# Performance work log

Hardware: AMD Instinct MI355X
Metric: run time of the kernel (lower is better)

The kernel has to match this reference:

```python
import jax, jax.numpy as jnp
import numpy as np


def setup_inputs() -> dict:
    key = jax.random.key(0)
    ks = jax.random.split(key, 6)
    B, C, H, W, K = 4, 64, 352, 1216, 3
    OC = K * K - 1  # 8 guide channels from convbn
    return {
        "feature": jax.random.normal(ks[0], (B, C, H, W), jnp.float32),
        "conv_w": jax.random.normal(ks[1], (OC, C, 3, 3), jnp.float32) * 0.05,
        "gamma": jax.random.uniform(ks[2], (OC,), jnp.float32, 0.5, 1.5),
        "beta": jax.random.normal(ks[3], (OC,), jnp.float32) * 0.1,
        "mean": jax.random.normal(ks[4], (OC,), jnp.float32) * 0.1,
        "var": jax.random.uniform(ks[5], (OC,), jnp.float32, 0.5, 1.5),
        "kernel_size": K,
    }


def reference(feature, conv_w, gamma, beta, mean, var, kernel_size):
    k = kernel_size
    eps = 1e-5
    # conv 3x3, stride 1, pad 1, no bias  -> [B, k*k-1, H, W]
    x = jax.lax.conv_general_dilated(
        feature, conv_w, window_strides=(1, 1), padding=((1, 1), (1, 1)),
        dimension_numbers=("NCHW", "OIHW", "NCHW"))
    c = lambda v: v[None, :, None, None]
    # BatchNorm2d in eval mode (running stats + affine)
    guide = (x - c(mean)) * (c(gamma) * jax.lax.rsqrt(c(var) + eps)) + c(beta)
    # L1-normalize across channels, middle weight = 1 - sum of the others
    gsum = jnp.sum(jnp.abs(guide), axis=1, keepdims=True)
    guide = guide / gsum
    guide_mid = 1.0 - jnp.sum(guide, axis=1, keepdims=True)
    mid = (k * k - 1) // 2
    # per-offset zero-pad each single channel into [H+k-1, W+k-1] canvas
    pads = []
    for t in range(k * k):  # fixed small loop over kernel offsets (k*k = 9)
        i, j = t // k, t % k  # top=i, bottom=k-1-i, left=j, right=k-1-j
        if t < mid:
            ch = guide[:, t:t + 1]
        elif t > mid:
            ch = guide[:, t - 1:t]
        else:
            ch = guide_mid
        pads.append(jnp.pad(ch, ((0, 0), (0, 0), (i, k - 1 - i), (j, k - 1 - j))))
    return jnp.concatenate(pads, axis=1)  # [B, k*k, H+k-1, W+k-1]
```

## Files before the change

### kernel.cpp

```cpp
#include <hip/hip_runtime.h>
#include <hip/hip_bf16.h>

#define BATCH 4
#define CIN 64
#define HH 352
#define WW 1216
#define OCH 8
#define OHH 354
#define OWW 1218
#define HW (HH * WW)

#define BH 16
#define BW 32
#define FR 18
#define FC 34
#define NPOS (FR * FC)
#define NTHR 256
#define NIT 10
#define GX 38
#define GY 22
#define NWG (GX * GY * BATCH)
#define CPX (NWG / 8)

typedef short bf16x8 __attribute__((ext_vector_type(8)));
typedef float f32x4  __attribute__((ext_vector_type(4)));

static __device__ __forceinline__ unsigned f2bf(float x) {
    unsigned u = __float_as_uint(x);
    return (u + 0x7FFFu + ((u >> 16) & 1u)) >> 16;
}

__global__ void repack_kernel(const float* __restrict__ conv_w,
                              const float* __restrict__ gamma,
                              const float* __restrict__ beta,
                              const float* __restrict__ mean,
                              const float* __restrict__ var,
                              unsigned short* __restrict__ wB,
                              float* __restrict__ bias)
{
    int tid = blockIdx.x * 256 + threadIdx.x;
    if (tid < 18 * 64) {
        int tc = tid >> 6;
        int lane = tid & 63;
        int tap = tc >> 1, cc = tc & 1;
        int oc = lane & 15, hi = lane >> 4;
        unsigned v[8];
#pragma unroll
        for (int j = 0; j < 8; ++j) {
            float w = 0.f;
            if (oc < 8) {
                int c = cc * 32 + hi * 8 + j;
                float scl = gamma[oc] * rsqrtf(var[oc] + 1e-5f);
                w = conv_w[((size_t)oc * CIN + c) * 9 + tap] * scl;
            }
            v[j] = f2bf(w);
        }
        uint4 pk;
        pk.x = v[0] | (v[1] << 16);
        pk.y = v[2] | (v[3] << 16);
        pk.z = v[4] | (v[5] << 16);
        pk.w = v[6] | (v[7] << 16);
        ((uint4*)wB)[tid] = pk;
    }
    if (tid < OCH) {
        float scl = gamma[tid] * rsqrtf(var[tid] + 1e-5f);
        bias[tid] = beta[tid] - mean[tid] * scl;
    }
}

__global__ void border_kernel(float* __restrict__ out)
{
    const int bt = blockIdx.x;
    const int t = bt % 9;
    const int i = t / 3, j = t % 3;
    float* pl = out + (size_t)bt * OHH * OWW;
    const int r0 = (i == 0) ? HH : 0;
    const int r1 = (i == 2) ? 1 : (OHH - 1);
    const int c0 = (j == 0) ? WW : 0;
    const int c1 = (j == 2) ? 1 : (OWW - 1);
    const int nrow = 2 * OWW;
    for (int idx = threadIdx.x; idx < 2 * OWW + 2 * OHH; idx += blockDim.x) {
        if (idx < nrow) {
            int r = (idx < OWW) ? r0 : r1;
            int c = (idx < OWW) ? idx : idx - OWW;
            pl[(size_t)r * OWW + c] = 0.f;
        } else {
            int k = idx - nrow;
            int c = (k < OHH) ? c0 : c1;
            int r = (k < OHH) ? k : k - OHH;
            pl[(size_t)r * OWW + c] = 0.f;
        }
    }
}

__global__ __launch_bounds__(NTHR, 2)
void conv_mfma(const float* __restrict__ feature,
               const unsigned short* __restrict__ wB,
               const float* __restrict__ bias,
               float* __restrict__ out)
{
    __shared__ uint4 sF[NPOS * 4];

    const int lin = blockIdx.x;
    const int wg  = (lin & 7) * CPX + (lin >> 3);
    const int bx  = wg % GX;
    const int byz = wg / GX;
    const int by  = byz % GY;
    const int b   = byz / GY;

    const int tid  = threadIdx.x;
    const int wave = tid >> 6;
    const int lane = tid & 63;
    const int oc   = lane & 15;
    const int hi   = lane >> 4;
    const int h0 = by * BH;
    const int w0 = bx * BW;

    const float* fb = feature + (size_t)b * CIN * HW;
    const int soct = tid & 3;
    const int p0   = tid >> 2;

    f32x4 acc[4][2];
#pragma unroll
    for (int rr = 0; rr < 4; ++rr)
#pragma unroll
        for (int cg = 0; cg < 2; ++cg) acc[rr][cg] = (f32x4)0.f;

#pragma unroll 1
    for (int cc = 0; cc < 2; ++cc) {
        if (cc) __syncthreads();
        const float* chbase = fb + (size_t)(cc * 32 + soct * 8) * HW;
        float v[NIT][8];
        float msk[NIT];
        int   cps[NIT];
#pragma unroll
        for (int it = 0; it < NIT; ++it) {
            int pos = p0 + it * 64;
            int cp = (pos < NPOS) ? pos : (NPOS - 1);
            int fr = cp / FC;
            int fc = cp - fr * FC;
            int gh = h0 - 1 + fr, gw = w0 - 1 + fc;
            bool ok = ((unsigned)gh < (unsigned)HH) && ((unsigned)gw < (unsigned)WW);
            int sgh = min(max(gh, 0), HH - 1);
            int sgw = min(max(gw, 0), WW - 1);
            const float* sp = chbase + sgh * WW + sgw;
#pragma unroll
            for (int j = 0; j < 8; ++j) v[it][j] = sp[(size_t)j * HW];
            msk[it] = ok ? 1.f : 0.f;
            cps[it] = cp;
        }
        bf16x8 bwl[9];
#pragma unroll
        for (int t = 0; t < 9; ++t)
            bwl[t] = ((const bf16x8*)wB)[(t * 2 + cc) * 64 + lane];
#pragma unroll
        for (int it = 0; it < NIT; ++it) {
            float mk = msk[it];
            uint4 pk;
            pk.x = f2bf(v[it][0] * mk) | (f2bf(v[it][1] * mk) << 16);
            pk.y = f2bf(v[it][2] * mk) | (f2bf(v[it][3] * mk) << 16);
            pk.z = f2bf(v[it][4] * mk) | (f2bf(v[it][5] * mk) << 16);
            pk.w = f2bf(v[it][6] * mk) | (f2bf(v[it][7] * mk) << 16);
            int cp = cps[it];
            sF[cp * 4 + (soct ^ ((cp >> 1) & 3))] = pk;
        }
        __syncthreads();
#pragma unroll
        for (int t = 0; t < 9; ++t) {
            const int dh = t / 3, dw = t % 3;
#pragma unroll
            for (int rr = 0; rr < 4; ++rr) {
                const int fr = wave * 4 + rr + dh;
#pragma unroll
                for (int cg = 0; cg < 2; ++cg) {
                    const int fc = cg * 16 + oc + dw;
                    const int pp = fr * FC + fc;
                    bf16x8 av = *reinterpret_cast<const bf16x8*>(&sF[pp * 4 + (hi ^ ((pp >> 1) & 3))]);
                    acc[rr][cg] = __builtin_amdgcn_mfma_f32_16x16x32_bf16(av, bwl[t], acc[rr][cg], 0, 0, 0);
                }
            }
        }
    }

    const float myb = (oc < 8) ? bias[oc] : 0.f;
    const int t = (oc < 8) ? ((oc < 4) ? oc : oc + 1) : 4;
    const bool dow = (oc <= 8);
    const int ii = t / 3, jj = t % 3;
    float* pl = out + ((size_t)(b * 9 + t) * OHH + ii) * OWW + jj;

#pragma unroll
    for (int rr = 0; rr < 4; ++rr) {
        const int h = h0 + wave * 4 + rr;
#pragma unroll
        for (int cg = 0; cg < 2; ++cg) {
#pragma unroll
            for (int reg = 0; reg < 4; ++reg) {
                float vv = acc[rr][cg][reg] + myb;
                float av = fabsf(vv);
                float sv = vv;
                av += __shfl_xor(av, 1);  sv += __shfl_xor(sv, 1);
                av += __shfl_xor(av, 2);  sv += __shfl_xor(sv, 2);
                av += __shfl_xor(av, 4);  sv += __shfl_xor(sv, 4);
                av += __shfl_xor(av, 8);  sv += __shfl_xor(sv, 8);
                float inv = 1.0f / av;
                float val = (oc == 8) ? (1.0f - sv * inv) : (vv * inv);
                if (dow) {
                    int w = w0 + cg * 16 + hi * 4 + reg;
                    pl[(size_t)h * OWW + w] = val;
                }
            }
        }
    }
}

extern "C" void kernel_launch(void* const* d_in, const int* in_sizes, int n_in,
                              void* d_out, int out_size, void* d_ws, size_t ws_size,
                              hipStream_t stream) {
    const float* feature = (const float*)d_in[0];
    const float* conv_w  = (const float*)d_in[1];
    const float* gamma   = (const float*)d_in[2];
    const float* beta    = (const float*)d_in[3];
    const float* mean    = (const float*)d_in[4];
    const float* var     = (const float*)d_in[5];
    float* out = (float*)d_out;

    unsigned short* wB = (unsigned short*)d_ws;
    float* bias = (float*)((char*)d_ws + 18432);

    border_kernel<<<BATCH * 9, 256, 0, stream>>>(out);
    repack_kernel<<<5, 256, 0, stream>>>(conv_w, gamma, beta, mean, var, wB, bias);
    conv_mfma<<<NWG, NTHR, 0, stream>>>(feature, wB, bias, out);
}
```

Measured before the change: 219.9 us.

## Give each wave a private LDS halo tile and drop block barriers

Each wave now stages its own 6-row halo window (its 4 output rows plus 2 halo rows) into a private LDS slot, so the two __syncthreads per channel chunk are removed. Loads are split into three smaller passes to cap register use. The cost is redundant global reads and bf16 conversion of overlapping halo rows (6 rows per 4 instead of 18 per 16), plus more LDS per block, which may reduce occupancy.

```diff
diff --git a/kernel.cpp b/kernel.cpp
--- a/kernel.cpp
+++ b/kernel.cpp
@@ -12,11 +12,11 @@
 
 #define BH 16
 #define BW 32
-#define FR 18
 #define FC 34
-#define NPOS (FR * FC)
+#define WROWS 6
+#define WPOS (WROWS * FC)
+#define WSLOT (WPOS * 4)
 #define NTHR 256
-#define NIT 10
 #define GX 38
 #define GY 22
 #define NWG (GX * GY * BATCH)
@@ -93,13 +93,37 @@
     }
 }
 
+#define STAGE_PASS(Q0, NP) { \
+    float v[NP][8]; float mk[NP]; int sl[NP]; \
+    _Pragma("unroll") for (int k = 0; k < NP; ++k) { \
+        int pos = p0 + (Q0 + k) * 16; \
+        pos = (pos < WPOS) ? pos : (WPOS - 1);           \
+        int lr = pos / FC; int fc = pos - lr * FC; \
+        int gh = h0w - 1 + lr, gw = w0 - 1 + fc; \
+        bool ok = ((unsigned)gh < (unsigned)HH) && ((unsigned)gw < (unsigned)WW); \
+        int sgh = min(max(gh, 0), HH - 1); \
+        int sgw = min(max(gw, 0), WW - 1); \
+        const float* sp = chbase + sgh * WW + sgw; \
+        _Pragma("unroll") for (int j = 0; j < 8; ++j) v[k][j] = sp[(size_t)j * HW]; \
+        mk[k] = ok ? 1.f : 0.f; \
+        sl[k] = wslot0 + pos * 4 + (soct ^ ((pos >> 1) & 3)); \
+    } \
+    _Pragma("unroll") for (int k = 0; k < NP; ++k) { \
+        float m_ = mk[k]; uint4 pk; \
+        pk.x = f2bf(v[k][0] * m_) | (f2bf(v[k][1] * m_) << 16); \
+        pk.y = f2bf(v[k][2] * m_) | (f2bf(v[k][3] * m_) << 16); \
+        pk.z = f2bf(v[k][4] * m_) | (f2bf(v[k][5] * m_) << 16); \
+        pk.w = f2bf(v[k][6] * m_) | (f2bf(v[k][7] * m_) << 16); \
+        sF[sl[k]] = pk; \
+    } }
+
 __global__ __launch_bounds__(NTHR, 2)
 void conv_mfma(const float* __restrict__ feature,
                const unsigned short* __restrict__ wB,
                const float* __restrict__ bias,
                float* __restrict__ out)
 {
-    __shared__ uint4 sF[NPOS * 4];
+    __shared__ uint4 sF[4 * WSLOT];
 
     const int lin = blockIdx.x;
     const int wg  = (lin & 7) * CPX + (lin >> 3);
@@ -115,10 +139,12 @@
     const int hi   = lane >> 4;
     const int h0 = by * BH;
     const int w0 = bx * BW;
+    const int h0w = h0 + wave * 4;
+    const int wslot0 = wave * WSLOT;
 
     const float* fb = feature + (size_t)b * CIN * HW;
-    const int soct = tid & 3;
-    const int p0   = tid >> 2;
+    const int soct = lane & 3;
+    const int p0   = lane >> 2;
 
     f32x4 acc[4][2];
 #pragma unroll
@@ -128,54 +154,29 @@
 
 #pragma unroll 1
     for (int cc = 0; cc < 2; ++cc) {
-        if (cc) __syncthreads();
         const float* chbase = fb + (size_t)(cc * 32 + soct * 8) * HW;
-        float v[NIT][8];
-        float msk[NIT];
-        int   cps[NIT];
-#pragma unroll
-        for (int it = 0; it < NIT; ++it) {
-            int pos = p0 + it * 64;
-            int cp = (pos < NPOS) ? pos : (NPOS - 1);
-            int fr = cp / FC;
-            int fc = cp - fr * FC;
-            int gh = h0 - 1 + fr, gw = w0 - 1 + fc;
-            bool ok = ((unsigned)gh < (unsigned)HH) && ((unsigned)gw < (unsigned)WW);
-            int sgh = min(max(gh, 0), HH - 1);
-            int sgw = min(max(gw, 0), WW - 1);
-            const float* sp = chbase + sgh * WW + sgw;
-#pragma unroll
-            for (int j = 0; j < 8; ++j) v[it][j] = sp[(size_t)j * HW];
-            msk[it] = ok ? 1.f : 0.f;
-            cps[it] = cp;
-        }
+
+        STAGE_PASS(0, 5)
+        STAGE_PASS(5, 4)
+        STAGE_PASS(9, 4)
+
         bf16x8 bwl[9];
 #pragma unroll
         for (int t = 0; t < 9; ++t)
             bwl[t] = ((const bf16x8*)wB)[(t * 2 + cc) * 64 + lane];
-#pragma unroll
-        for (int it = 0; it < NIT; ++it) {
-            float mk = msk[it];
-            uint4 pk;
-            pk.x = f2bf(v[it][0] * mk) | (f2bf(v[it][1] * mk) << 16);
-            pk.y = f2bf(v[it][2] * mk) | (f2bf(v[it][3] * mk) << 16);
-            pk.z = f2bf(v[it][4] * mk) | (f2bf(v[it][5] * mk) << 16);
-            pk.w = f2bf(v[it][6] * mk) | (f2bf(v[it][7] * mk) << 16);
-            int cp = cps[it];
-            sF[cp * 4 + (soct ^ ((cp >> 1) & 3))] = pk;
-        }
-        __syncthreads();
+
 #pragma unroll
         for (int t = 0; t < 9; ++t) {
             const int dh = t / 3, dw = t % 3;
 #pragma unroll
             for (int rr = 0; rr < 4; ++rr) {
-                const int fr = wave * 4 + rr + dh;
+                const int lr = rr + dh;
 #pragma unroll
                 for (int cg = 0; cg < 2; ++cg) {
                     const int fc = cg * 16 + oc + dw;
-                    const int pp = fr * FC + fc;
-                    bf16x8 av = *reinterpret_cast<const bf16x8*>(&sF[pp * 4 + (hi ^ ((pp >> 1) & 3))]);
+                    const int pp = lr * FC + fc;
+                    bf16x8 av = *reinterpret_cast<const bf16x8*>(
+                        &sF[wslot0 + pp * 4 + (hi ^ ((pp >> 1) & 3))]);
                     acc[rr][cg] = __builtin_amdgcn_mfma_f32_16x16x32_bf16(av, bwl[t], acc[rr][cg], 0, 0, 0);
                 }
             }
@@ -190,7 +191,7 @@
 
 #pragma unroll
     for (int rr = 0; rr < 4; ++rr) {
-        const int h = h0 + wave * 4 + rr;
+        const int h = h0w + rr;
 #pragma unroll
         for (int cg = 0; cg < 2; ++cg) {
 #pragma unroll
```

Result: slower. 263.7 us (+19.9%).

## Double-buffer LDS and prefetch second channel chunk during first MFMA pass

Applied to the files above, without the earlier changes.

The conv kernel now keeps two LDS buffers, one per 32-channel chunk. The first chunk is loaded in two halves and staged, then the global loads for the second chunk are issued into registers before the first chunk's MFMAs run, so memory latency overlaps with compute. The second chunk is packed into the other buffer afterwards, which removes one barrier. In exchange the kernel holds 80 floats of prefetch in registers during the MFMA loop and doubles LDS use, which may cause spills or lower occupancy under launch_bounds(256,2).

```diff
diff --git a/kernel.cpp b/kernel.cpp
--- a/kernel.cpp
+++ b/kernel.cpp
@@ -93,13 +93,34 @@
     }
 }
 
+#define PACK1(VV, MK, SL, BUF) { \
+    uint4 pk_; \
+    pk_.x = f2bf(VV[0] * MK) | (f2bf(VV[1] * MK) << 16); \
+    pk_.y = f2bf(VV[2] * MK) | (f2bf(VV[3] * MK) << 16); \
+    pk_.z = f2bf(VV[4] * MK) | (f2bf(VV[5] * MK) << 16); \
+    pk_.w = f2bf(VV[6] * MK) | (f2bf(VV[7] * MK) << 16); \
+    (BUF)[SL] = pk_; }
+
+#define MFMA_CHUNK(BUF) \
+    _Pragma("unroll") for (int t = 0; t < 9; ++t) { \
+        const int dh = t / 3, dw = t % 3; \
+        _Pragma("unroll") for (int rr = 0; rr < 4; ++rr) { \
+            const int fr = wv4 + rr + dh; \
+            _Pragma("unroll") for (int cg = 0; cg < 2; ++cg) { \
+                const int fc = cg * 16 + oc + dw; \
+                const int pp = fr * FC + fc; \
+                bf16x8 av = *reinterpret_cast<const bf16x8*>(&(BUF)[pp * 4 + (hi ^ ((pp >> 1) & 3))]); \
+                acc[rr][cg] = __builtin_amdgcn_mfma_f32_16x16x32_bf16(av, bwl[t], acc[rr][cg], 0, 0, 0); \
+            } } }
+
 __global__ __launch_bounds__(NTHR, 2)
 void conv_mfma(const float* __restrict__ feature,
                const unsigned short* __restrict__ wB,
                const float* __restrict__ bias,
                float* __restrict__ out)
 {
-    __shared__ uint4 sF[NPOS * 4];
+    __shared__ uint4 sA[NPOS * 4];
+    __shared__ uint4 sB[NPOS * 4];
 
     const int lin = blockIdx.x;
     const int wg  = (lin & 7) * CPX + (lin >> 3);
@@ -113,6 +134,7 @@
     const int lane = tid & 63;
     const int oc   = lane & 15;
     const int hi   = lane >> 4;
+    const int wv4  = wave * 4;
     const int h0 = by * BH;
     const int w0 = bx * BW;
 
@@ -126,60 +148,64 @@
 #pragma unroll
         for (int cg = 0; cg < 2; ++cg) acc[rr][cg] = (f32x4)0.f;
 
+    {
+        const float* chbase = fb + (size_t)(soct * 8) * HW;
 #pragma unroll 1
-    for (int cc = 0; cc < 2; ++cc) {
-        if (cc) __syncthreads();
-        const float* chbase = fb + (size_t)(cc * 32 + soct * 8) * HW;
-        float v[NIT][8];
-        float msk[NIT];
-        int   cps[NIT];
+        for (int hf = 0; hf < 2; ++hf) {
+            float v[5][8]; float mk5[5]; int sl5[5];
+#pragma unroll
+            for (int k = 0; k < 5; ++k) {
+                int it = hf * 5 + k;
+                int pos2 = p0 + it * 64; pos2 = (pos2 < NPOS) ? pos2 : (NPOS - 1);
+                int fr2 = pos2 / FC; int fc2 = pos2 - fr2 * FC;
+                int gh2 = h0 - 1 + fr2, gw2 = w0 - 1 + fc2;
+                mk5[k] = (((unsigned)gh2 < (unsigned)HH) && ((unsigned)gw2 < (unsigned)WW)) ? 1.f : 0.f;
+                sl5[k] = pos2 * 4 + (soct ^ ((pos2 >> 1) & 3));
+                const float* sp2 = chbase + (min(max(gh2, 0), HH - 1) * WW + min(max(gw2, 0), WW - 1));
+#pragma unroll
+                for (int j = 0; j < 8; ++j) v[k][j] = sp2[(size_t)j * HW];
+            }
+#pragma unroll
+            for (int k = 0; k < 5; ++k) PACK1(v[k], mk5[k], sl5[k], sA)
+        }
+    }
+    __syncthreads();
+
+    float v1[NIT][8]; float mk1[NIT]; int sl1[NIT];
+    {
+        const float* chbase = fb + (size_t)(32 + soct * 8) * HW;
 #pragma unroll
         for (int it = 0; it < NIT; ++it) {
-            int pos = p0 + it * 64;
-            int cp = (pos < NPOS) ? pos : (NPOS - 1);
-            int fr = cp / FC;
-            int fc = cp - fr * FC;
-            int gh = h0 - 1 + fr, gw = w0 - 1 + fc;
-            bool ok = ((unsigned)gh < (unsigned)HH) && ((unsigned)gw < (unsigned)WW);
-            int sgh = min(max(gh, 0), HH - 1);
-            int sgw = min(max(gw, 0), WW - 1);
-            const float* sp = chbase + sgh * WW + sgw;
-#pragma unroll
-            for (int j = 0; j < 8; ++j) v[it][j] = sp[(size_t)j * HW];
-            msk[it] = ok ? 1.f : 0.f;
-            cps[it] = cp;
-        }
+            int pos2 = p0 + it * 64; pos2 = (pos2 < NPOS) ? pos2 : (NPOS - 1);
+            int fr2 = pos2 / FC; int fc2 = pos2 - fr2 * FC;
+            int gh2 = h0 - 1 + fr2, gw2 = w0 - 1 + fc2;
+            mk1[it] = (((unsigned)gh2 < (unsigned)HH) && ((unsigned)gw2 < (unsigned)WW)) ? 1.f : 0.f;
+            sl1[it] = pos2 * 4 + (soct ^ ((pos2 >> 1) & 3));
+            const float* sp2 = chbase + (min(max(gh2, 0), HH - 1) * WW + min(max(gw2, 0), WW - 1));
+#pragma unroll
+            for (int j = 0; j < 8; ++j) v1[it][j] = sp2[(size_t)j * HW];
+        }
+    }
+    __builtin_amdgcn_sched_barrier(0);
+
+    {
         bf16x8 bwl[9];
 #pragma unroll
         for (int t = 0; t < 9; ++t)
-            bwl[t] = ((const bf16x8*)wB)[(t * 2 + cc) * 64 + lane];
-#pragma unroll
-        for (int it = 0; it < NIT; ++it) {
-            float mk = msk[it];
-            uint4 pk;
-            pk.x = f2bf(v[it][0] * mk) | (f2bf(v[it][1] * mk) << 16);
-            pk.y = f2bf(v[it][2] * mk) | (f2bf(v[it][3] * mk) << 16);
-            pk.z = f2bf(v[it][4] * mk) | (f2bf(v[it][5] * mk) << 16);
-            pk.w = f2bf(v[it][6] * mk) | (f2bf(v[it][7] * mk) << 16);
-            int cp = cps[it];
-            sF[cp * 4 + (soct ^ ((cp >> 1) & 3))] = pk;
-        }
-        __syncthreads();
-#pragma unroll
-        for (int t = 0; t < 9; ++t) {
-            const int dh = t / 3, dw = t % 3;
-#pragma unroll
-            for (int rr = 0; rr < 4; ++rr) {
-                const int fr = wave * 4 + rr + dh;
-#pragma unroll
-                for (int cg = 0; cg < 2; ++cg) {
-                    const int fc = cg * 16 + oc + dw;
-                    const int pp = fr * FC + fc;
-                    bf16x8 av = *reinterpret_cast<const bf16x8*>(&sF[pp * 4 + (hi ^ ((pp >> 1) & 3))]);
-                    acc[rr][cg] = __builtin_amdgcn_mfma_f32_16x16x32_bf16(av, bwl[t], acc[rr][cg], 0, 0, 0);
-                }
-            }
-        }
+            bwl[t] = ((const bf16x8*)wB)[(t * 2 + 0) * 64 + lane];
+        MFMA_CHUNK(sA)
+    }
+
+#pragma unroll
+    for (int it = 0; it < NIT; ++it) PACK1(v1[it], mk1[it], sl1[it], sB)
+    __syncthreads();
+
+    {
+        bf16x8 bwl[9];
+#pragma unroll
+        for (int t = 0; t < 9; ++t)
+            bwl[t] = ((const bf16x8*)wB)[(t * 2 + 1) * 64 + lane];
+        MFMA_CHUNK(sB)
     }
 
     const float myb = (oc < 8) ? bias[oc] : 0.f;
@@ -190,7 +216,7 @@
 
 #pragma unroll
     for (int rr = 0; rr < 4; ++rr) {
-        const int h = h0 + wave * 4 + rr;
+        const int h = h0 + wv4 + rr;
 #pragma unroll
         for (int cg = 0; cg < 2; ++cg) {
 #pragma unroll
```

After: 225.1 us. +2.4%, slower.

## Widen conv tile to 64 columns with 512 threads and 16-channel MFMA chunks

Applied to the files above, without the earlier changes.

Doubles the work-group tile width to 64 columns with 8 waves, which cuts the halo overhead and the number of work-groups. Input channels are now staged in four 16-channel chunks using 16x16x16 bf16 MFMA instead of two 32-channel chunks with 16x16x32. The per-position address and mask math is hoisted out of the channel loop, and the LDS swizzle is dropped. More barriers, twice as many MFMA instructions, and possible LDS bank conflicts are the trade-offs.

```diff
diff --git a/kernel.cpp b/kernel.cpp
--- a/kernel.cpp
+++ b/kernel.cpp
@@ -11,19 +11,31 @@
 #define HW (HH * WW)
 
 #define BH 16
-#define BW 32
+#define BW 64
 #define FR 18
-#define FC 34
+#define FC 66
 #define NPOS (FR * FC)
-#define NTHR 256
-#define NIT 10
-#define GX 38
+#define NTHR 512
+#define NIT 5
+#define GX 19
 #define GY 22
 #define NWG (GX * GY * BATCH)
 #define CPX (NWG / 8)
 
-typedef short bf16x8 __attribute__((ext_vector_type(8)));
+typedef short bf16x4 __attribute__((ext_vector_type(4)));
 typedef float f32x4  __attribute__((ext_vector_type(4)));
+
+#if defined(__HIP_DEVICE_COMPILE__)
+#if __has_builtin(__builtin_amdgcn_mfma_f32_16x16x16bf16_1k)
+#define MFMA16(A, B, C) __builtin_amdgcn_mfma_f32_16x16x16bf16_1k(A, B, C, 0, 0, 0)
+#elif __has_builtin(__builtin_amdgcn_mfma_f32_16x16x16_bf16)
+#define MFMA16(A, B, C) __builtin_amdgcn_mfma_f32_16x16x16_bf16(A, B, C, 0, 0, 0)
+#else
+#error "no 16x16x16 bf16 mfma builtin on device"
+#endif
+#else
+#define MFMA16(A, B, C) (C)
+#endif
 
 static __device__ __forceinline__ unsigned f2bf(float x) {
     unsigned u = __float_as_uint(x);
@@ -39,28 +51,26 @@
                               float* __restrict__ bias)
 {
     int tid = blockIdx.x * 256 + threadIdx.x;
-    if (tid < 18 * 64) {
+    if (tid < 36 * 64) {
         int tc = tid >> 6;
         int lane = tid & 63;
-        int tap = tc >> 1, cc = tc & 1;
+        int tap = tc >> 2, q = tc & 3;
         int oc = lane & 15, hi = lane >> 4;
-        unsigned v[8];
-#pragma unroll
-        for (int j = 0; j < 8; ++j) {
+        unsigned v[4];
+#pragma unroll
+        for (int j = 0; j < 4; ++j) {
             float w = 0.f;
             if (oc < 8) {
-                int c = cc * 32 + hi * 8 + j;
+                int c = q * 16 + hi * 4 + j;
                 float scl = gamma[oc] * rsqrtf(var[oc] + 1e-5f);
                 w = conv_w[((size_t)oc * CIN + c) * 9 + tap] * scl;
             }
             v[j] = f2bf(w);
         }
-        uint4 pk;
+        uint2 pk;
         pk.x = v[0] | (v[1] << 16);
         pk.y = v[2] | (v[3] << 16);
-        pk.z = v[4] | (v[5] << 16);
-        pk.w = v[6] | (v[7] << 16);
-        ((uint4*)wB)[tid] = pk;
+        ((uint2*)wB)[tid] = pk;
     }
     if (tid < OCH) {
         float scl = gamma[tid] * rsqrtf(var[tid] + 1e-5f);
@@ -99,7 +109,7 @@
                const float* __restrict__ bias,
                float* __restrict__ out)
 {
-    __shared__ uint4 sF[NPOS * 4];
+    __shared__ uint4 sF[NPOS * 2];
 
     const int lin = blockIdx.x;
     const int wg  = (lin & 7) * CPX + (lin >> 3);
@@ -113,12 +123,28 @@
     const int lane = tid & 63;
     const int oc   = lane & 15;
     const int hi   = lane >> 4;
+    const int hb   = (wave >> 1) * 4;
+    const int wb   = (wave & 1) * 32;
     const int h0 = by * BH;
     const int w0 = bx * BW;
 
     const float* fb = feature + (size_t)b * CIN * HW;
-    const int soct = tid & 3;
-    const int p0   = tid >> 2;
+    const int soct = tid & 1;
+    const int p0   = tid >> 1;
+
+    int   off[NIT], sl[NIT];
+    float mk[NIT];
+#pragma unroll
+    for (int it = 0; it < NIT; ++it) {
+        int pos = p0 + it * 256;
+        pos = (pos < NPOS) ? pos : (NPOS - 1);
+        int fr = pos / FC;
+        int fc = pos - fr * FC;
+        int gh = h0 - 1 + fr, gw = w0 - 1 + fc;
+        mk[it] = (((unsigned)gh < (unsigned)HH) && ((unsigned)gw < (unsigned)WW)) ? 1.f : 0.f;
+        off[it] = min(max(gh, 0), HH - 1) * WW + min(max(gw, 0), WW - 1);
+        sl[it]  = pos * 2 + soct;
+    }
 
     f32x4 acc[4][2];
 #pragma unroll
@@ -127,56 +153,47 @@
         for (int cg = 0; cg < 2; ++cg) acc[rr][cg] = (f32x4)0.f;
 
 #pragma unroll 1
-    for (int cc = 0; cc < 2; ++cc) {
-        if (cc) __syncthreads();
-        const float* chbase = fb + (size_t)(cc * 32 + soct * 8) * HW;
+    for (int q = 0; q < 4; ++q) {
+        if (q) __syncthreads();
+        const float* chbase = fb + (size_t)(q * 16 + soct * 8) * HW;
+
         float v[NIT][8];
-        float msk[NIT];
-        int   cps[NIT];
 #pragma unroll
         for (int it = 0; it < NIT; ++it) {
-            int pos = p0 + it * 64;
-            int cp = (pos < NPOS) ? pos : (NPOS - 1);
-            int fr = cp / FC;
-            int fc = cp - fr * FC;
-            int gh = h0 - 1 + fr, gw = w0 - 1 + fc;
-            bool ok = ((unsigned)gh < (unsigned)HH) && ((unsigned)gw < (unsigned)WW);
-            int sgh = min(max(gh, 0), HH - 1);
-            int sgw = min(max(gw, 0), WW - 1);
-            const float* sp = chbase + sgh * WW + sgw;
+            const float* sp = chbase + off[it];
 #pragma unroll
             for (int j = 0; j < 8; ++j) v[it][j] = sp[(size_t)j * HW];
-            msk[it] = ok ? 1.f : 0.f;
-            cps[it] = cp;
-        }
-        bf16x8 bwl[9];
+        }
+#pragma unroll
+        for (int it = 0; it < NIT; ++it) {
+            float m_ = mk[it];
+            uint4 pk;
+            pk.x = f2bf(v[it][0] * m_) | (f2bf(v[it][1] * m_) << 16);
+            pk.y = f2bf(v[it][2] * m_) | (f2bf(v[it][3] * m_) << 16);
+            pk.z = f2bf(v[it][4] * m_) | (f2bf(v[it][5] * m_) << 16);
+            pk.w = f2bf(v[it][6] * m_) | (f2bf(v[it][7] * m_) << 16);
+            sF[sl[it]] = pk;
+        }
+        __syncthreads();
+
+        bf16x4 bwl[9];
 #pragma unroll
         for (int t = 0; t < 9; ++t)
-            bwl[t] = ((const bf16x8*)wB)[(t * 2 + cc) * 64 + lane];
-#pragma unroll
-        for (int it = 0; it < NIT; ++it) {
-            float mk = msk[it];
-            uint4 pk;
-            pk.x = f2bf(v[it][0] * mk) | (f2bf(v[it][1] * mk) << 16);
-            pk.y = f2bf(v[it][2] * mk) | (f2bf(v[it][3] * mk) << 16);
-            pk.z = f2bf(v[it][4] * mk) | (f2bf(v[it][5] * mk) << 16);
-            pk.w = f2bf(v[it][6] * mk) | (f2bf(v[it][7] * mk) << 16);
-            int cp = cps[it];
-            sF[cp * 4 + (soct ^ ((cp >> 1) & 3))] = pk;
-        }
-        __syncthreads();
+            bwl[t] = ((const bf16x4*)wB)[(t * 4 + q) * 64 + lane];
+
 #pragma unroll
         for (int t = 0; t < 9; ++t) {
             const int dh = t / 3, dw = t % 3;
 #pragma unroll
             for (int rr = 0; rr < 4; ++rr) {
-                const int fr = wave * 4 + rr + dh;
+                const int fr = hb + rr + dh;
 #pragma unroll
                 for (int cg = 0; cg < 2; ++cg) {
-                    const int fc = cg * 16 + oc + dw;
+                    const int fc = wb + cg * 16 + oc + dw;
                     const int pp = fr * FC + fc;
-                    bf16x8 av = *reinterpret_cast<const bf16x8*>(&sF[pp * 4 + (hi ^ ((pp >> 1) & 3))]);
-                    acc[rr][cg] = __builtin_amdgcn_mfma_f32_16x16x32_bf16(av, bwl[t], acc[rr][cg], 0, 0, 0);
+                    bf16x4 av = *reinterpret_cast<const bf16x4*>(
+                        (const short*)sF + pp * 16 + hi * 4);
+                    acc[rr][cg] = MFMA16(av, bwl[t], acc[rr][cg]);
                 }
             }
         }
@@ -190,7 +207,7 @@
 
 #pragma unroll
     for (int rr = 0; rr < 4; ++rr) {
-        const int h = h0 + wave * 4 + rr;
+        const int h = h0 + hb + rr;
 #pragma unroll
         for (int cg = 0; cg < 2; ++cg) {
 #pragma unroll
@@ -205,7 +222,7 @@
                 float inv = 1.0f / av;
                 float val = (oc == 8) ? (1.0f - sv * inv) : (vv * inv);
                 if (dow) {
-                    int w = w0 + cg * 16 + hi * 4 + reg;
+                    int w = w0 + wb + cg * 16 + hi * 4 + reg;
                     pl[(size_t)h * OWW + w] = val;
                 }
             }
@@ -228,6 +245,6 @@
     float* bias = (float*)((char*)d_ws + 18432);
 
     border_kernel<<<BATCH * 9, 256, 0, stream>>>(out);
-    repack_kernel<<<5, 256, 0, stream>>>(conv_w, gamma, beta, mean, var, wB, bias);
+    repack_kernel<<<9, 256, 0, stream>>>(conv_w, gamma, beta, mean, var, wB, bias);
     conv_mfma<<<NWG, NTHR, 0, stream>>>(feature, wB, bias, out);
 }
```

After: 246.4 us. 1.12x slower.
